# Kernel tuning notes

Measured on AMD Instinct MI355X. Metric: run time of the kernel, lower is better.

The kernel has to match this reference:

```python
import jax, jax.numpy as jnp
import numpy as np

V, E, H, L, B, S = 32000, 512, 512, 2, 8, 512


def setup_inputs() -> dict:
    key = jax.random.key(0)
    ks = jax.random.split(key, 16)
    emb = jax.random.normal(ks[0], (V, E), jnp.float32) * 0.02
    emb = emb.at[0].set(0.0)  # padding_idx=0
    init_state = jax.random.normal(ks[1], (2, L, H), jnp.float32)  # [h;c] params
    def xav(k, shp):
        fan_in, fan_out = shp[1], shp[0]
        lim = np.sqrt(6.0 / (fan_in + fan_out)).astype(np.float32)
        return jax.random.uniform(k, shp, jnp.float32, -lim, lim)
    inp = {
        'emb_table': emb,
        'init_state': init_state,
        'w_ih0': xav(ks[2], (4 * H, E)), 'w_hh0': xav(ks[3], (4 * H, H)),
        'b_ih0': jnp.zeros((4 * H,), jnp.float32), 'b_hh0': jnp.zeros((4 * H,), jnp.float32),
        'w_ih1': xav(ks[4], (4 * H, H)), 'w_hh1': xav(ks[5], (4 * H, H)),
        'b_ih1': jnp.zeros((4 * H,), jnp.float32), 'b_hh1': jnp.zeros((4 * H,), jnp.float32),
        'wg': xav(ks[6], (2 * H, H)), 'bg': jnp.zeros((2 * H,), jnp.float32),
        'wd': xav(ks[7], (V, H)), 'bd': jnp.zeros((V,), jnp.float32),
        'eps': jax.random.normal(ks[8], (B, S, H), jnp.float32),
        'x': jax.random.randint(ks[9], (B, S), 0, V, jnp.int64),
    }
    return inp


def _lstm_layer(xs, h0, c0, w_ih, w_hh, b_ih, b_hh):
    # xs: [S, B, in]; returns hidden sequence [S, B, H]
    b = b_ih + b_hh
    def step(carry, x_t):
        h, c = carry
        gates = x_t @ w_ih.T + h @ w_hh.T + b  # [B, 4H]
        i, f, g, o = jnp.split(gates, 4, axis=-1)  # torch gate order i,f,g,o
        c = jax.nn.sigmoid(f) * c + jax.nn.sigmoid(i) * jnp.tanh(g)
        h = jax.nn.sigmoid(o) * jnp.tanh(c)
        return (h, c), h
    _, hs = jax.lax.scan(step, (h0, c0), xs)
    return hs


def reference(emb_table, init_state, w_ih0, w_hh0, b_ih0, b_hh0,
              w_ih1, w_hh1, b_ih1, b_hh1, wg, bg, wd, bd, eps, x):
    Bsz = x.shape[0]
    embedding = emb_table[x]  # [B, S, E]
    h0 = jnp.broadcast_to(init_state[0][:, None, :], (L, Bsz, H))
    c0 = jnp.broadcast_to(init_state[1][:, None, :], (L, Bsz, H))
    xs = embedding.transpose(1, 0, 2)  # time-major [S, B, E]
    hs0 = _lstm_layer(xs, h0[0], c0[0], w_ih0, w_hh0, b_ih0, b_hh0)
    hs1 = _lstm_layer(hs0, h0[1], c0[1], w_ih1, w_hh1, b_ih1, b_hh1)
    out = hs1.transpose(1, 0, 2)  # [B, S, H]
    stats = out @ wg.T + bg  # [B, S, 2H]
    std = jax.nn.softplus(stats[:, :, :H])  # diagonal of covariance matrix
    mu = stats[:, :, H:]
    # MultivariateNormal(mu, cov=diag(std)).rsample() => mu + sqrt(std) * eps
    sample = mu + jnp.sqrt(std) * eps
    logits = sample @ wd.T + bd  # [B, S, V]
    return (logits, mu, std)
```

## Files before the change

kernel.cpp:

```cpp
#include <hip/hip_runtime.h>


typedef __attribute__((ext_vector_type(4))) float f32x4;
typedef __attribute__((ext_vector_type(8))) short short8;
typedef __attribute__((ext_vector_type(4))) unsigned short u16x4;

#define V_SZ 32000
#define E_SZ 512
#define H_SZ 512
#define B_SZ 8
#define S_SZ 512
#define NTOK 4096
#define G4H  2048

__device__ __forceinline__ unsigned short f2bf(float x) {
  unsigned int b = __float_as_uint(x);
  b += 0x7FFFu + ((b >> 16) & 1u);
  return (unsigned short)(b >> 16);
}
__device__ __forceinline__ float bf2f(unsigned short u) {
  return __uint_as_float(((unsigned int)u) << 16);
}

__device__ __forceinline__ void split4(const f32x4 v, u16x4& hv, u16x4& lv) {
  unsigned short h0 = f2bf(v.x); lv.x = f2bf(v.x - bf2f(h0)); hv.x = h0;
  unsigned short h1 = f2bf(v.y); lv.y = f2bf(v.y - bf2f(h1)); hv.y = h1;
  unsigned short h2 = f2bf(v.z); lv.z = f2bf(v.z - bf2f(h2)); hv.z = h2;
  unsigned short h3 = f2bf(v.w); lv.w = f2bf(v.w - bf2f(h3)); hv.w = h3;
}

__global__ void split_kernel(const float* __restrict__ src,
                             unsigned short* __restrict__ hi,
                             unsigned short* __restrict__ lo, int n4) {
  int i = blockIdx.x * 256 + threadIdx.x;
  if (i >= n4) return;
  f32x4 v = ((const f32x4*)src)[i];
  u16x4 hv, lv;
  split4(v, hv, lv);
  ((u16x4*)hi)[i] = hv;
  ((u16x4*)lo)[i] = lv;
}

__global__ void bias_sum_kernel(const float* __restrict__ a0, const float* __restrict__ c0,
                                const float* __restrict__ a1, const float* __restrict__ c1,
                                float* __restrict__ o0, float* __restrict__ o1) {
  int i = blockIdx.x * 256 + threadIdx.x;
  if (i < G4H) { o0[i] = a0[i] + c0[i]; o1[i] = a1[i] + c1[i]; }
}

__global__ void embed_split_kernel(const float* __restrict__ emb, const int* __restrict__ x,
                                   unsigned short* __restrict__ hi, unsigned short* __restrict__ lo) {
  int gid = blockIdx.x * 256 + threadIdx.x;
  int r = gid >> 7;
  int kq = (gid & 127) << 2;
  int tok = x[r];
  f32x4 v = *(const f32x4*)(emb + (size_t)tok * E_SZ + kq);
  u16x4 hv, lv;
  split4(v, hv, lv);
  *(u16x4*)(hi + (size_t)r * E_SZ + kq) = hv;
  *(u16x4*)(lo + (size_t)r * E_SZ + kq) = lv;
}

__device__ __forceinline__ int swz32(int row, int seg) {
  return row * 32 + (((seg ^ (row & 3)) << 3));
}

__global__ __launch_bounds__(256, 2) void gemm3_kernel(
    const unsigned short* __restrict__ Ah, const unsigned short* __restrict__ Al,
    const unsigned short* __restrict__ Bh, const unsigned short* __restrict__ Bl,
    const float* __restrict__ bias, float* __restrict__ C,
    int M, int N, int K) {
  __shared__ unsigned short sAh[128 * 32];
  __shared__ unsigned short sAl[128 * 32];
  __shared__ unsigned short sBh[128 * 32];
  __shared__ unsigned short sBl[128 * 32];

  const int t = threadIdx.x;
  const int lane = t & 63;
  const int wave = t >> 6;
  const int wr = wave >> 1, wc = wave & 1;
  const size_t m0 = (size_t)blockIdx.y * 128;
  const size_t n0 = (size_t)blockIdx.x * 128;

  f32x4 acc[4][4];
#pragma unroll
  for (int i = 0; i < 4; ++i)
#pragma unroll
    for (int j = 0; j < 4; ++j) acc[i][j] = (f32x4){0.f, 0.f, 0.f, 0.f};

  const int r0 = t >> 2;
  const int seg0 = t & 3;

  const int nk = K >> 5;
  for (int ks = 0; ks < nk; ++ks) {
    const int k0 = ks << 5;
    short8 vAh[2], vAl[2], vBh[2], vBl[2];
#pragma unroll
    for (int r = 0; r < 2; ++r) {
      int row = r0 + r * 64;
      size_t ga = (m0 + row) * (size_t)K + k0 + seg0 * 8;
      size_t gb = (n0 + row) * (size_t)K + k0 + seg0 * 8;
      vAh[r] = *(const short8*)(Ah + ga);
      vAl[r] = *(const short8*)(Al + ga);
      vBh[r] = *(const short8*)(Bh + gb);
      vBl[r] = *(const short8*)(Bl + gb);
    }
    __syncthreads();
#pragma unroll
    for (int r = 0; r < 2; ++r) {
      int row = r0 + r * 64;
      int d = swz32(row, seg0);
      *(short8*)(sAh + d) = vAh[r];
      *(short8*)(sAl + d) = vAl[r];
      *(short8*)(sBh + d) = vBh[r];
      *(short8*)(sBl + d) = vBl[r];
    }
    __syncthreads();

    short8 ah[4], al[4], bh[4], bl[4];
    const int seg = lane >> 4;
#pragma unroll
    for (int m = 0; m < 4; ++m) {
      int row = wr * 64 + m * 16 + (lane & 15);
      int d = swz32(row, seg);
      ah[m] = *(const short8*)(sAh + d);
      al[m] = *(const short8*)(sAl + d);
    }
#pragma unroll
    for (int n = 0; n < 4; ++n) {
      int row = wc * 64 + n * 16 + (lane & 15);
      int d = swz32(row, seg);
      bh[n] = *(const short8*)(sBh + d);
      bl[n] = *(const short8*)(sBl + d);
    }
#pragma unroll
    for (int m = 0; m < 4; ++m) {
#pragma unroll
      for (int n = 0; n < 4; ++n) {
        acc[m][n] = __builtin_amdgcn_mfma_f32_16x16x32_bf16(ah[m], bh[n], acc[m][n], 0, 0, 0);
        acc[m][n] = __builtin_amdgcn_mfma_f32_16x16x32_bf16(ah[m], bl[n], acc[m][n], 0, 0, 0);
        acc[m][n] = __builtin_amdgcn_mfma_f32_16x16x32_bf16(al[m], bh[n], acc[m][n], 0, 0, 0);
      }
    }
  }

#pragma unroll
  for (int m = 0; m < 4; ++m) {
#pragma unroll
    for (int n = 0; n < 4; ++n) {
      size_t gr0 = m0 + wr * 64 + m * 16 + ((lane >> 4) << 2);
      size_t gc = n0 + wc * 64 + n * 16 + (lane & 15);
      float bv = bias ? bias[gc] : 0.f;
#pragma unroll
      for (int j = 0; j < 4; ++j) {
        C[(gr0 + j) * (size_t)N + gc] = acc[m][n][j] + bv;
      }
    }
  }
}

#define SEQ_NB 192
#define SEQ_NB_L0 64

__device__ __forceinline__ float sigm(float x) { return 1.f / (1.f + expf(-x)); }

__global__ __launch_bounds__(256, 1) void lstm_seq_kernel(
    const float* __restrict__ gx0,
    const float* __restrict__ w_hh0,
    const float* __restrict__ w_ih1,
    const float* __restrict__ w_hh1,
    const float* __restrict__ b1s,
    const float* __restrict__ initst,
    float* __restrict__ h0_all,
    float* __restrict__ h1_all,
    unsigned short* __restrict__ hs1h,
    unsigned short* __restrict__ hs1l,
    unsigned int* __restrict__ sig0,
    unsigned int* __restrict__ sig1) {
  const int blk = blockIdx.x;
  const int t = threadIdx.x;
  const bool isL1 = (blk >= SEQ_NB_L0);
  const int lb = isL1 ? (blk - SEQ_NB_L0) : blk;

  __shared__ float hA[8][512];
  __shared__ float hB[8][512];
  __shared__ float gates_s[32][8];

  const int tb = t >> 7;
  const int rg = isL1 ? ((t >> 5) & 3) : ((t >> 4) & 7);
  const int kg = isL1 ? (t & 31) : (t & 15);

  f32x4 w[4][8];
  if (!isL1) {
#pragma unroll
    for (int rr = 0; rr < 4; ++rr) {
      int rl = rg * 4 + rr;
      int grow = (rl >> 3) * H_SZ + lb * 8 + (rl & 7);
      const float* src = w_hh0 + (size_t)grow * H_SZ + kg * 4;
#pragma unroll
      for (int j = 0; j < 8; ++j) w[rr][j] = *(const f32x4*)(src + j * 64);
    }
  } else {
#pragma unroll
    for (int rr = 0; rr < 4; ++rr) {
      int rl = rg * 4 + rr;
      int grow = (rl >> 2) * H_SZ + lb * 4 + (rl & 3);
      const float* s1 = w_ih1 + (size_t)grow * H_SZ + kg * 4;
      const float* s2 = w_hh1 + (size_t)grow * H_SZ + kg * 4;
#pragma unroll
      for (int j = 0; j < 4; ++j) w[rr][j] = *(const f32x4*)(s1 + j * 128);
#pragma unroll
      for (int j = 0; j < 4; ++j) w[rr][4 + j] = *(const f32x4*)(s2 + j * 128);
    }
  }

  const int UPB = isL1 ? 4 : 8;
  const int nCell = UPB * 8;
  const int cu = t >> 3, cb = t & 7;
  const int cunit = lb * UPB + cu;
  float creg = 0.f;
  float bgi = 0.f, bgf = 0.f, bgg = 0.f, bgo = 0.f;
  if (t < nCell) {
    creg = initst[1024 + (isL1 ? 512 : 0) + cunit];
    if (isL1) {
      bgi = b1s[cunit];
      bgf = b1s[512 + cunit];
      bgg = b1s[1024 + cunit];
      bgo = b1s[1536 + cunit];
    }
  }

  for (int step = 0; step < 512; ++step) {
    float pgi = 0.f, pgf = 0.f, pgg = 0.f, pgo = 0.f;
    if (!isL1 && t < nCell) {
      const float* gx = gx0 + ((size_t)(cb * S_SZ + step)) * G4H + cunit;
      pgi = gx[0];
      pgf = gx[512];
      pgg = gx[1024];
      pgo = gx[1536];
    }

    if (t < 64) {
      if (!isL1) {
        if (step > 0) {
          const unsigned int* s0 = sig0 + (size_t)(step - 1) * 64;
          while (true) {
            unsigned int v = __hip_atomic_load(&s0[t], __ATOMIC_RELAXED, __HIP_MEMORY_SCOPE_AGENT);
            if (__all(v != 0)) break;
            __builtin_amdgcn_s_sleep(1);
          }
        }
      } else {
        const unsigned int* s0 = sig0 + (size_t)step * 64;
        const unsigned int* s1 = (step > 0) ? (sig1 + (size_t)(step - 1) * 128) : nullptr;
        while (true) {
          int ok = (__hip_atomic_load(&s0[t], __ATOMIC_RELAXED, __HIP_MEMORY_SCOPE_AGENT) != 0);
          if (s1) {
            ok &= (__hip_atomic_load(&s1[t], __ATOMIC_RELAXED, __HIP_MEMORY_SCOPE_AGENT) != 0);
            ok &= (__hip_atomic_load(&s1[64 + t], __ATOMIC_RELAXED, __HIP_MEMORY_SCOPE_AGENT) != 0);
          }
          if (__all(ok)) break;
          __builtin_amdgcn_s_sleep(1);
        }
      }
    }
    __syncthreads();

    if (!isL1) {
      const float* src = (step == 0) ? (initst) : (h0_all + (size_t)(step - 1) * 4096);
      if (step == 0) {
#pragma unroll
        for (int i = 0; i < 4; ++i) {
          int idx = t + i * 256;
          int b = idx >> 7;
          int kc = (idx & 127) << 2;
          *(f32x4*)&hA[b][kc] = *(const f32x4*)(initst + kc);
        }
      } else {
#pragma unroll
        for (int i = 0; i < 4; ++i) {
          int idx = t + i * 256;
          int b = idx >> 7;
          int kc = (idx & 127) << 2;
          *(f32x4*)&hA[b][kc] = *(const f32x4*)(src + b * H_SZ + kc);
        }
      }
    } else {
      const float* s0 = h0_all + (size_t)step * 4096;
      const float* s1 = (step == 0) ? nullptr : (h1_all + (size_t)(step - 1) * 4096);
#pragma unroll
      for (int i = 0; i < 4; ++i) {
        int idx = t + i * 256;
        int b = idx >> 7;
        int kc = (idx & 127) << 2;
        *(f32x4*)&hA[b][kc] = *(const f32x4*)(s0 + b * H_SZ + kc);
        f32x4 v1 = s1 ? *(const f32x4*)(s1 + b * H_SZ + kc)
                      : *(const f32x4*)(initst + 512 + kc);
        *(f32x4*)&hB[b][kc] = v1;
      }
    }
    __syncthreads();

    float acc[4][4];
#pragma unroll
    for (int rr = 0; rr < 4; ++rr)
#pragma unroll
      for (int bq = 0; bq < 4; ++bq) acc[rr][bq] = 0.f;

    if (!isL1) {
#pragma unroll
      for (int bq = 0; bq < 4; ++bq) {
        const float* hb = &hA[tb * 4 + bq][0];
#pragma unroll
        for (int j = 0; j < 8; ++j) {
          f32x4 hq = *(const f32x4*)(hb + kg * 4 + j * 64);
#pragma unroll
          for (int rr = 0; rr < 4; ++rr)
            acc[rr][bq] += w[rr][j].x * hq.x + w[rr][j].y * hq.y +
                           w[rr][j].z * hq.z + w[rr][j].w * hq.w;
        }
      }
#pragma unroll
      for (int s = 1; s < 16; s <<= 1) {
#pragma unroll
        for (int rr = 0; rr < 4; ++rr)
#pragma unroll
          for (int bq = 0; bq < 4; ++bq)
            acc[rr][bq] += __shfl_xor(acc[rr][bq], s, 64);
      }
      if (kg == 0) {
#pragma unroll
        for (int rr = 0; rr < 4; ++rr)
#pragma unroll
          for (int bq = 0; bq < 4; ++bq)
            gates_s[rg * 4 + rr][tb * 4 + bq] = acc[rr][bq];
      }
    } else {
#pragma unroll
      for (int bq = 0; bq < 4; ++bq) {
        const int b = tb * 4 + bq;
        const float* ha = &hA[b][0];
        const float* hbp = &hB[b][0];
#pragma unroll
        for (int j = 0; j < 4; ++j) {
          f32x4 hq = *(const f32x4*)(ha + kg * 4 + j * 128);
#pragma unroll
          for (int rr = 0; rr < 4; ++rr)
            acc[rr][bq] += w[rr][j].x * hq.x + w[rr][j].y * hq.y +
                           w[rr][j].z * hq.z + w[rr][j].w * hq.w;
        }
#pragma unroll
        for (int j = 0; j < 4; ++j) {
          f32x4 hq = *(const f32x4*)(hbp + kg * 4 + j * 128);
#pragma unroll
          for (int rr = 0; rr < 4; ++rr)
            acc[rr][bq] += w[rr][4 + j].x * hq.x + w[rr][4 + j].y * hq.y +
                           w[rr][4 + j].z * hq.z + w[rr][4 + j].w * hq.w;
        }
      }
#pragma unroll
      for (int s = 1; s < 32; s <<= 1) {
#pragma unroll
        for (int rr = 0; rr < 4; ++rr)
#pragma unroll
          for (int bq = 0; bq < 4; ++bq)
            acc[rr][bq] += __shfl_xor(acc[rr][bq], s, 64);
      }
      if (kg == 0) {
#pragma unroll
        for (int rr = 0; rr < 4; ++rr)
#pragma unroll
          for (int bq = 0; bq < 4; ++bq)
            gates_s[rg * 4 + rr][tb * 4 + bq] = acc[rr][bq];
      }
    }
    __syncthreads();

    if (t < nCell) {
      float gi, gf, gg, go;
      if (!isL1) {
        gi = gates_s[cu][cb] + pgi;
        gf = gates_s[8 + cu][cb] + pgf;
        gg = gates_s[16 + cu][cb] + pgg;
        go = gates_s[24 + cu][cb] + pgo;
      } else {
        gi = gates_s[cu][cb] + bgi;
        gf = gates_s[4 + cu][cb] + bgf;
        gg = gates_s[8 + cu][cb] + bgg;
        go = gates_s[12 + cu][cb] + bgo;
      }
      float cn = sigm(gf) * creg + sigm(gi) * tanhf(gg);
      float h = sigm(go) * tanhf(cn);
      creg = cn;
      if (!isL1) {
        __hip_atomic_store(&h0_all[(size_t)step * 4096 + cb * H_SZ + cunit], h,
                           __ATOMIC_RELAXED, __HIP_MEMORY_SCOPE_AGENT);
      } else {
        __hip_atomic_store(&h1_all[(size_t)step * 4096 + cb * H_SZ + cunit], h,
                           __ATOMIC_RELAXED, __HIP_MEMORY_SCOPE_AGENT);
        size_t r = (size_t)(cb * S_SZ + step) * H_SZ + cunit;
        unsigned short hh = f2bf(h);
        hs1h[r] = hh;
        hs1l[r] = f2bf(h - bf2f(hh));
      }
    }
    if (t == 0) {
      asm volatile("s_waitcnt vmcnt(0)" ::: "memory");
      unsigned int* slot = isL1 ? (sig1 + (size_t)step * 128 + lb)
                                : (sig0 + (size_t)step * 64 + lb);
      __hip_atomic_store(slot, 1u, __ATOMIC_RELAXED, __HIP_MEMORY_SCOPE_AGENT);
    }
  }
}

__global__ void sample_kernel(const float* __restrict__ stats, const float* __restrict__ eps,
                              unsigned short* __restrict__ sh, unsigned short* __restrict__ sl,
                              float* __restrict__ omu, float* __restrict__ ostd) {
  int gid = blockIdx.x * 256 + threadIdx.x;
  int r = gid >> 9, hh = gid & 511;
  float sp = stats[(size_t)r * 1024 + hh];
  float mu = stats[(size_t)r * 1024 + 512 + hh];
  float sd = (sp > 20.f) ? sp : log1pf(expf(sp));
  float smp = mu + sqrtf(sd) * eps[gid];
  omu[gid] = mu;
  ostd[gid] = sd;
  unsigned short h = f2bf(smp);
  sh[gid] = h;
  sl[gid] = f2bf(smp - bf2f(h));
}

extern "C" void kernel_launch(void* const* d_in, const int* in_sizes, int n_in,
                              void* d_out, int out_size, void* d_ws, size_t ws_size,
                              hipStream_t stream) {
  const float* emb    = (const float*)d_in[0];
  const float* initst = (const float*)d_in[1];
  const float* w_ih0  = (const float*)d_in[2];
  const float* w_hh0  = (const float*)d_in[3];
  const float* b_ih0  = (const float*)d_in[4];
  const float* b_hh0  = (const float*)d_in[5];
  const float* w_ih1  = (const float*)d_in[6];
  const float* w_hh1  = (const float*)d_in[7];
  const float* b_ih1  = (const float*)d_in[8];
  const float* b_hh1  = (const float*)d_in[9];
  const float* wg     = (const float*)d_in[10];
  const float* bg     = (const float*)d_in[11];
  const float* wd     = (const float*)d_in[12];
  const float* bd     = (const float*)d_in[13];
  const float* eps    = (const float*)d_in[14];
  const int*   x      = (const int*)d_in[15];

  char* ws = (char*)d_ws;
  size_t off = 0;
  auto alloc = [&](size_t sz) {
    void* p = ws + off;
    off = (off + sz + 255) & ~(size_t)255;
    return p;
  };
  unsigned int* sig0     = (unsigned int*)alloc((size_t)512 * 64 * 4);
  unsigned int* sig1     = (unsigned int*)alloc((size_t)512 * 128 * 4);
  float* b0s             = (float*)alloc(G4H * 4);
  float* b1s             = (float*)alloc(G4H * 4);
  unsigned short* wih0h  = (unsigned short*)alloc((size_t)G4H * E_SZ * 2);
  unsigned short* wih0l  = (unsigned short*)alloc((size_t)G4H * E_SZ * 2);
  unsigned short* wgh    = (unsigned short*)alloc((size_t)1024 * H_SZ * 2);
  unsigned short* wgl    = (unsigned short*)alloc((size_t)1024 * H_SZ * 2);
  unsigned short* wdh    = (unsigned short*)alloc((size_t)V_SZ * H_SZ * 2);
  unsigned short* wdl    = (unsigned short*)alloc((size_t)V_SZ * H_SZ * 2);
  unsigned short* a0h    = (unsigned short*)alloc((size_t)NTOK * E_SZ * 2);
  unsigned short* a0l    = (unsigned short*)alloc((size_t)NTOK * E_SZ * 2);
  float* gx0             = (float*)alloc((size_t)NTOK * G4H * 4);
  float* h0_all          = (float*)alloc((size_t)512 * 4096 * 4);
  float* h1_all          = (float*)alloc((size_t)512 * 4096 * 4);
  unsigned short* hs1h   = (unsigned short*)alloc((size_t)NTOK * H_SZ * 2);
  unsigned short* hs1l   = (unsigned short*)alloc((size_t)NTOK * H_SZ * 2);
  float* stats           = (float*)alloc((size_t)NTOK * 1024 * 4);
  unsigned short* smph   = (unsigned short*)alloc((size_t)NTOK * H_SZ * 2);
  unsigned short* smpl   = (unsigned short*)alloc((size_t)NTOK * H_SZ * 2);

  float* out_logits = (float*)d_out;
  float* out_mu     = out_logits + (size_t)NTOK * V_SZ;
  float* out_std    = out_mu + (size_t)NTOK * H_SZ;

  (void)hipMemsetAsync(sig0, 0, (size_t)512 * 64 * 4, stream);
  (void)hipMemsetAsync(sig1, 0, (size_t)512 * 128 * 4, stream);

  split_kernel<<<(G4H * E_SZ / 4 + 255) / 256, 256, 0, stream>>>(w_ih0, wih0h, wih0l, G4H * E_SZ / 4);
  split_kernel<<<(1024 * H_SZ / 4 + 255) / 256, 256, 0, stream>>>(wg, wgh, wgl, 1024 * H_SZ / 4);
  split_kernel<<<(V_SZ * H_SZ / 4 + 255) / 256, 256, 0, stream>>>(wd, wdh, wdl, V_SZ * H_SZ / 4);
  bias_sum_kernel<<<8, 256, 0, stream>>>(b_ih0, b_hh0, b_ih1, b_hh1, b0s, b1s);

  embed_split_kernel<<<NTOK * 128 / 256, 256, 0, stream>>>(emb, x, a0h, a0l);

  gemm3_kernel<<<dim3(G4H / 128, NTOK / 128), 256, 0, stream>>>(
      a0h, a0l, wih0h, wih0l, b0s, gx0, NTOK, G4H, E_SZ);

  lstm_seq_kernel<<<SEQ_NB, 256, 0, stream>>>(
      gx0, w_hh0, w_ih1, w_hh1, b1s, initst, h0_all, h1_all, hs1h, hs1l, sig0, sig1);

  gemm3_kernel<<<dim3(1024 / 128, NTOK / 128), 256, 0, stream>>>(
      hs1h, hs1l, wgh, wgl, bg, stats, NTOK, 1024, H_SZ);

  sample_kernel<<<NTOK * H_SZ / 256, 256, 0, stream>>>(stats, eps, smph, smpl, out_mu, out_std);

  gemm3_kernel<<<dim3(V_SZ / 128, NTOK / 128), 256, 0, stream>>>(
      smph, smpl, wdh, wdl, bd, out_logits, NTOK, V_SZ, H_SZ);
}
```

Before: 3.789 ms.

## Split layer-1 LSTM into separate input-projection and recurrent block groups

Layer 1 was computed by 128 blocks, each doing both the w_ih1·h0 and w_hh1·h1 products per step. The new scheme uses three groups of 64 blocks: layer-0 recurrence, a layer-1 input-projection group that computes w_ih1·h0[t] as soon as layer 0 finishes step t and publishes the result with per-block flags, and a layer-1 recurrent group that only does w_hh1·h1. This takes the input projection off the layer-1 critical path so it overlaps with the recurrence. The cost is an extra global round trip through gx1 and another level of flag synchronization per step.

```diff
diff --git a/kernel.cpp b/kernel.cpp
--- a/kernel.cpp
+++ b/kernel.cpp
@@ -160,7 +160,6 @@
 }
 
 #define SEQ_NB 192
-#define SEQ_NB_L0 64
 
 __device__ __forceinline__ float sigm(float x) { return 1.f / (1.f + expf(-x)); }
 
@@ -173,56 +172,43 @@
     const float* __restrict__ initst,
     float* __restrict__ h0_all,
     float* __restrict__ h1_all,
+    float* __restrict__ gx1,
     unsigned short* __restrict__ hs1h,
     unsigned short* __restrict__ hs1l,
     unsigned int* __restrict__ sig0,
-    unsigned int* __restrict__ sig1) {
+    unsigned int* __restrict__ sig1,
+    unsigned int* __restrict__ sig1a) {
   const int blk = blockIdx.x;
   const int t = threadIdx.x;
-  const bool isL1 = (blk >= SEQ_NB_L0);
-  const int lb = isL1 ? (blk - SEQ_NB_L0) : blk;
+  const int grp = blk >> 6;
+  const int lb = blk & 63;
 
   __shared__ float hA[8][512];
-  __shared__ float hB[8][512];
   __shared__ float gates_s[32][8];
 
   const int tb = t >> 7;
-  const int rg = isL1 ? ((t >> 5) & 3) : ((t >> 4) & 7);
-  const int kg = isL1 ? (t & 31) : (t & 15);
-
+  const int rg = (t >> 4) & 7;
+  const int kg = t & 15;
+
+  const float* wsrc = (grp == 0) ? w_hh0 : (grp == 1) ? w_ih1 : w_hh1;
   f32x4 w[4][8];
-  if (!isL1) {
-#pragma unroll
-    for (int rr = 0; rr < 4; ++rr) {
-      int rl = rg * 4 + rr;
-      int grow = (rl >> 3) * H_SZ + lb * 8 + (rl & 7);
-      const float* src = w_hh0 + (size_t)grow * H_SZ + kg * 4;
-#pragma unroll
-      for (int j = 0; j < 8; ++j) w[rr][j] = *(const f32x4*)(src + j * 64);
-    }
-  } else {
-#pragma unroll
-    for (int rr = 0; rr < 4; ++rr) {
-      int rl = rg * 4 + rr;
-      int grow = (rl >> 2) * H_SZ + lb * 4 + (rl & 3);
-      const float* s1 = w_ih1 + (size_t)grow * H_SZ + kg * 4;
-      const float* s2 = w_hh1 + (size_t)grow * H_SZ + kg * 4;
-#pragma unroll
-      for (int j = 0; j < 4; ++j) w[rr][j] = *(const f32x4*)(s1 + j * 128);
-#pragma unroll
-      for (int j = 0; j < 4; ++j) w[rr][4 + j] = *(const f32x4*)(s2 + j * 128);
-    }
+#pragma unroll
+  for (int rr = 0; rr < 4; ++rr) {
+    int rl = rg * 4 + rr;
+    int grow = (rl >> 3) * H_SZ + lb * 8 + (rl & 7);
+    const float* src = wsrc + (size_t)grow * H_SZ + kg * 4;
+#pragma unroll
+    for (int j = 0; j < 8; ++j) w[rr][j] = *(const f32x4*)(src + j * 64);
   }
 
-  const int UPB = isL1 ? 4 : 8;
-  const int nCell = UPB * 8;
   const int cu = t >> 3, cb = t & 7;
-  const int cunit = lb * UPB + cu;
+  const int cunit = lb * 8 + cu;
   float creg = 0.f;
   float bgi = 0.f, bgf = 0.f, bgg = 0.f, bgo = 0.f;
-  if (t < nCell) {
-    creg = initst[1024 + (isL1 ? 512 : 0) + cunit];
-    if (isL1) {
+  if (t < 64) {
+    if (grp == 0) creg = initst[1024 + cunit];
+    if (grp == 2) {
+      creg = initst[1024 + 512 + cunit];
       bgi = b1s[cunit];
       bgf = b1s[512 + cunit];
       bgg = b1s[1024 + cunit];
@@ -232,7 +218,7 @@
 
   for (int step = 0; step < 512; ++step) {
     float pgi = 0.f, pgf = 0.f, pgg = 0.f, pgo = 0.f;
-    if (!isL1 && t < nCell) {
+    if (grp == 0 && t < 64) {
       const float* gx = gx0 + ((size_t)(cb * S_SZ + step)) * G4H + cunit;
       pgi = gx[0];
       pgf = gx[512];
@@ -241,7 +227,7 @@
     }
 
     if (t < 64) {
-      if (!isL1) {
+      if (grp == 0) {
         if (step > 0) {
           const unsigned int* s0 = sig0 + (size_t)(step - 1) * 64;
           while (true) {
@@ -250,15 +236,19 @@
             __builtin_amdgcn_s_sleep(1);
           }
         }
+      } else if (grp == 1) {
+        const unsigned int* s0 = sig0 + (size_t)step * 64;
+        while (true) {
+          unsigned int v = __hip_atomic_load(&s0[t], __ATOMIC_RELAXED, __HIP_MEMORY_SCOPE_AGENT);
+          if (__all(v != 0)) break;
+          __builtin_amdgcn_s_sleep(1);
+        }
       } else {
-        const unsigned int* s0 = sig0 + (size_t)step * 64;
-        const unsigned int* s1 = (step > 0) ? (sig1 + (size_t)(step - 1) * 128) : nullptr;
+        const unsigned int* sa = sig1a + (size_t)step * 64 + lb;
+        const unsigned int* s1 = (step > 0) ? (sig1 + (size_t)(step - 1) * 64) : nullptr;
         while (true) {
-          int ok = (__hip_atomic_load(&s0[t], __ATOMIC_RELAXED, __HIP_MEMORY_SCOPE_AGENT) != 0);
-          if (s1) {
-            ok &= (__hip_atomic_load(&s1[t], __ATOMIC_RELAXED, __HIP_MEMORY_SCOPE_AGENT) != 0);
-            ok &= (__hip_atomic_load(&s1[64 + t], __ATOMIC_RELAXED, __HIP_MEMORY_SCOPE_AGENT) != 0);
-          }
+          int ok = (__hip_atomic_load(sa, __ATOMIC_RELAXED, __HIP_MEMORY_SCOPE_AGENT) != 0);
+          if (s1) ok &= (__hip_atomic_load(&s1[t], __ATOMIC_RELAXED, __HIP_MEMORY_SCOPE_AGENT) != 0);
           if (__all(ok)) break;
           __builtin_amdgcn_s_sleep(1);
         }
@@ -266,17 +256,19 @@
     }
     __syncthreads();
 
-    if (!isL1) {
-      const float* src = (step == 0) ? (initst) : (h0_all + (size_t)(step - 1) * 4096);
-      if (step == 0) {
-#pragma unroll
-        for (int i = 0; i < 4; ++i) {
-          int idx = t + i * 256;
-          int b = idx >> 7;
-          int kc = (idx & 127) << 2;
-          *(f32x4*)&hA[b][kc] = *(const f32x4*)(initst + kc);
-        }
-      } else {
+    float gxv[4];
+    if (grp == 2 && t < 64) {
+      const float* gp = gx1 + ((size_t)step * 64 + lb) * 256;
+#pragma unroll
+      for (int g = 0; g < 4; ++g) gxv[g] = gp[(g * 8 + cu) * 8 + cb];
+    }
+
+    {
+      const float* src;
+      if (grp == 0)       src = (step == 0) ? nullptr : (h0_all + (size_t)(step - 1) * 4096);
+      else if (grp == 1)  src = h0_all + (size_t)step * 4096;
+      else                src = (step == 0) ? nullptr : (h1_all + (size_t)(step - 1) * 4096);
+      if (src) {
 #pragma unroll
         for (int i = 0; i < 4; ++i) {
           int idx = t + i * 256;
@@ -284,50 +276,67 @@
           int kc = (idx & 127) << 2;
           *(f32x4*)&hA[b][kc] = *(const f32x4*)(src + b * H_SZ + kc);
         }
-      }
+      } else {
+        const float* ini = initst + (grp == 0 ? 0 : 512);
+#pragma unroll
+        for (int i = 0; i < 4; ++i) {
+          int idx = t + i * 256;
+          int b = idx >> 7;
+          int kc = (idx & 127) << 2;
+          *(f32x4*)&hA[b][kc] = *(const f32x4*)(ini + kc);
+        }
+      }
+    }
+    __syncthreads();
+
+    float acc[4][4];
+#pragma unroll
+    for (int rr = 0; rr < 4; ++rr)
+#pragma unroll
+      for (int bq = 0; bq < 4; ++bq) acc[rr][bq] = 0.f;
+#pragma unroll
+    for (int bq = 0; bq < 4; ++bq) {
+      const float* hb = &hA[tb * 4 + bq][0];
+#pragma unroll
+      for (int j = 0; j < 8; ++j) {
+        f32x4 hq = *(const f32x4*)(hb + kg * 4 + j * 64);
+#pragma unroll
+        for (int rr = 0; rr < 4; ++rr)
+          acc[rr][bq] += w[rr][j].x * hq.x + w[rr][j].y * hq.y +
+                         w[rr][j].z * hq.z + w[rr][j].w * hq.w;
+      }
+    }
+#pragma unroll
+    for (int s = 1; s < 16; s <<= 1) {
+#pragma unroll
+      for (int rr = 0; rr < 4; ++rr)
+#pragma unroll
+        for (int bq = 0; bq < 4; ++bq)
+          acc[rr][bq] += __shfl_xor(acc[rr][bq], s, 64);
+    }
+
+    if (grp == 1) {
+      if (kg == 0) {
+        unsigned long long* gq =
+            (unsigned long long*)(gx1 + ((size_t)step * 64 + lb) * 256);
+#pragma unroll
+        for (int rr = 0; rr < 4; ++rr) {
+          int rl = rg * 4 + rr;
+          unsigned long long lo =
+              ((unsigned long long)__float_as_uint(acc[rr][1]) << 32) |
+              (unsigned long long)__float_as_uint(acc[rr][0]);
+          unsigned long long hi =
+              ((unsigned long long)__float_as_uint(acc[rr][3]) << 32) |
+              (unsigned long long)__float_as_uint(acc[rr][2]);
+          __hip_atomic_store(&gq[rl * 4 + tb * 2], lo, __ATOMIC_RELAXED, __HIP_MEMORY_SCOPE_AGENT);
+          __hip_atomic_store(&gq[rl * 4 + tb * 2 + 1], hi, __ATOMIC_RELAXED, __HIP_MEMORY_SCOPE_AGENT);
+        }
+      }
+      __syncthreads();
+      if (t == 0)
+        __hip_atomic_store(&sig1a[(size_t)step * 64 + lb], 1u,
+                           __ATOMIC_RELAXED, __HIP_MEMORY_SCOPE_AGENT);
     } else {
-      const float* s0 = h0_all + (size_t)step * 4096;
-      const float* s1 = (step == 0) ? nullptr : (h1_all + (size_t)(step - 1) * 4096);
-#pragma unroll
-      for (int i = 0; i < 4; ++i) {
-        int idx = t + i * 256;
-        int b = idx >> 7;
-        int kc = (idx & 127) << 2;
-        *(f32x4*)&hA[b][kc] = *(const f32x4*)(s0 + b * H_SZ + kc);
-        f32x4 v1 = s1 ? *(const f32x4*)(s1 + b * H_SZ + kc)
-                      : *(const f32x4*)(initst + 512 + kc);
-        *(f32x4*)&hB[b][kc] = v1;
-      }
-    }
-    __syncthreads();
-
-    float acc[4][4];
-#pragma unroll
-    for (int rr = 0; rr < 4; ++rr)
-#pragma unroll
-      for (int bq = 0; bq < 4; ++bq) acc[rr][bq] = 0.f;
-
-    if (!isL1) {
-#pragma unroll
-      for (int bq = 0; bq < 4; ++bq) {
-        const float* hb = &hA[tb * 4 + bq][0];
-#pragma unroll
-        for (int j = 0; j < 8; ++j) {
-          f32x4 hq = *(const f32x4*)(hb + kg * 4 + j * 64);
-#pragma unroll
-          for (int rr = 0; rr < 4; ++rr)
-            acc[rr][bq] += w[rr][j].x * hq.x + w[rr][j].y * hq.y +
-                           w[rr][j].z * hq.z + w[rr][j].w * hq.w;
-        }
-      }
-#pragma unroll
-      for (int s = 1; s < 16; s <<= 1) {
-#pragma unroll
-        for (int rr = 0; rr < 4; ++rr)
-#pragma unroll
-          for (int bq = 0; bq < 4; ++bq)
-            acc[rr][bq] += __shfl_xor(acc[rr][bq], s, 64);
-      }
       if (kg == 0) {
 #pragma unroll
         for (int rr = 0; rr < 4; ++rr)
@@ -335,80 +344,42 @@
           for (int bq = 0; bq < 4; ++bq)
             gates_s[rg * 4 + rr][tb * 4 + bq] = acc[rr][bq];
       }
-    } else {
-#pragma unroll
-      for (int bq = 0; bq < 4; ++bq) {
-        const int b = tb * 4 + bq;
-        const float* ha = &hA[b][0];
-        const float* hbp = &hB[b][0];
-#pragma unroll
-        for (int j = 0; j < 4; ++j) {
-          f32x4 hq = *(const f32x4*)(ha + kg * 4 + j * 128);
-#pragma unroll
-          for (int rr = 0; rr < 4; ++rr)
-            acc[rr][bq] += w[rr][j].x * hq.x + w[rr][j].y * hq.y +
-                           w[rr][j].z * hq.z + w[rr][j].w * hq.w;
-        }
-#pragma unroll
-        for (int j = 0; j < 4; ++j) {
-          f32x4 hq = *(const f32x4*)(hbp + kg * 4 + j * 128);
-#pragma unroll
-          for (int rr = 0; rr < 4; ++rr)
-            acc[rr][bq] += w[rr][4 + j].x * hq.x + w[rr][4 + j].y * hq.y +
-                           w[rr][4 + j].z * hq.z + w[rr][4 + j].w * hq.w;
-        }
-      }
-#pragma unroll
-      for (int s = 1; s < 32; s <<= 1) {
-#pragma unroll
-        for (int rr = 0; rr < 4; ++rr)
-#pragma unroll
-          for (int bq = 0; bq < 4; ++bq)
-            acc[rr][bq] += __shfl_xor(acc[rr][bq], s, 64);
-      }
-      if (kg == 0) {
-#pragma unroll
-        for (int rr = 0; rr < 4; ++rr)
-#pragma unroll
-          for (int bq = 0; bq < 4; ++bq)
-            gates_s[rg * 4 + rr][tb * 4 + bq] = acc[rr][bq];
-      }
-    }
-    __syncthreads();
-
-    if (t < nCell) {
-      float gi, gf, gg, go;
-      if (!isL1) {
-        gi = gates_s[cu][cb] + pgi;
-        gf = gates_s[8 + cu][cb] + pgf;
-        gg = gates_s[16 + cu][cb] + pgg;
-        go = gates_s[24 + cu][cb] + pgo;
-      } else {
-        gi = gates_s[cu][cb] + bgi;
-        gf = gates_s[4 + cu][cb] + bgf;
-        gg = gates_s[8 + cu][cb] + bgg;
-        go = gates_s[12 + cu][cb] + bgo;
-      }
-      float cn = sigm(gf) * creg + sigm(gi) * tanhf(gg);
-      float h = sigm(go) * tanhf(cn);
-      creg = cn;
-      if (!isL1) {
-        __hip_atomic_store(&h0_all[(size_t)step * 4096 + cb * H_SZ + cunit], h,
-                           __ATOMIC_RELAXED, __HIP_MEMORY_SCOPE_AGENT);
-      } else {
-        __hip_atomic_store(&h1_all[(size_t)step * 4096 + cb * H_SZ + cunit], h,
-                           __ATOMIC_RELAXED, __HIP_MEMORY_SCOPE_AGENT);
-        size_t r = (size_t)(cb * S_SZ + step) * H_SZ + cunit;
-        unsigned short hh = f2bf(h);
-        hs1h[r] = hh;
-        hs1l[r] = f2bf(h - bf2f(hh));
-      }
-    }
-    if (t == 0) {
-      asm volatile("s_waitcnt vmcnt(0)" ::: "memory");
-      unsigned int* slot = isL1 ? (sig1 + (size_t)step * 128 + lb)
-                                : (sig0 + (size_t)step * 64 + lb);
-      __hip_atomic_store(slot, 1u, __ATOMIC_RELAXED, __HIP_MEMORY_SCOPE_AGENT);
+      __syncthreads();
+
+      if (t < 64) {
+        float gi, gf, gg, go;
+        if (grp == 0) {
+          gi = gates_s[cu][cb] + pgi;
+          gf = gates_s[8 + cu][cb] + pgf;
+          gg = gates_s[16 + cu][cb] + pgg;
+          go = gates_s[24 + cu][cb] + pgo;
+        } else {
+          gi = gates_s[cu][cb] + gxv[0] + bgi;
+          gf = gates_s[8 + cu][cb] + gxv[1] + bgf;
+          gg = gates_s[16 + cu][cb] + gxv[2] + bgg;
+          go = gates_s[24 + cu][cb] + gxv[3] + bgo;
+        }
+        float cn = sigm(gf) * creg + sigm(gi) * tanhf(gg);
+        float h = sigm(go) * tanhf(cn);
+        creg = cn;
+        if (grp == 0) {
+          __hip_atomic_store(&h0_all[(size_t)step * 4096 + cb * H_SZ + cunit], h,
+                             __ATOMIC_RELAXED, __HIP_MEMORY_SCOPE_AGENT);
+        } else {
+          __hip_atomic_store(&h1_all[(size_t)step * 4096 + cb * H_SZ + cunit], h,
+                             __ATOMIC_RELAXED, __HIP_MEMORY_SCOPE_AGENT);
+          size_t r = (size_t)(cb * S_SZ + step) * H_SZ + cunit;
+          unsigned short hh = f2bf(h);
+          hs1h[r] = hh;
+          hs1l[r] = f2bf(h - bf2f(hh));
+        }
+      }
+      if (t == 0) {
+        asm volatile("s_waitcnt vmcnt(0)" ::: "memory");
+        unsigned int* slot = (grp == 0) ? (sig0 + (size_t)step * 64 + lb)
+                                        : (sig1 + (size_t)step * 64 + lb);
+        __hip_atomic_store(slot, 1u, __ATOMIC_RELAXED, __HIP_MEMORY_SCOPE_AGENT);
+      }
     }
   }
 }
@@ -457,7 +428,8 @@
     return p;
   };
   unsigned int* sig0     = (unsigned int*)alloc((size_t)512 * 64 * 4);
-  unsigned int* sig1     = (unsigned int*)alloc((size_t)512 * 128 * 4);
+  unsigned int* sig1     = (unsigned int*)alloc((size_t)512 * 64 * 4);
+  unsigned int* sig1a    = (unsigned int*)alloc((size_t)512 * 64 * 4);
   float* b0s             = (float*)alloc(G4H * 4);
   float* b1s             = (float*)alloc(G4H * 4);
   unsigned short* wih0h  = (unsigned short*)alloc((size_t)G4H * E_SZ * 2);
@@ -469,6 +441,7 @@
   unsigned short* a0h    = (unsigned short*)alloc((size_t)NTOK * E_SZ * 2);
   unsigned short* a0l    = (unsigned short*)alloc((size_t)NTOK * E_SZ * 2);
   float* gx0             = (float*)alloc((size_t)NTOK * G4H * 4);
+  float* gx1             = (float*)alloc((size_t)512 * 64 * 256 * 4);
   float* h0_all          = (float*)alloc((size_t)512 * 4096 * 4);
   float* h1_all          = (float*)alloc((size_t)512 * 4096 * 4);
   unsigned short* hs1h   = (unsigned short*)alloc((size_t)NTOK * H_SZ * 2);
@@ -482,7 +455,8 @@
   float* out_std    = out_mu + (size_t)NTOK * H_SZ;
 
   (void)hipMemsetAsync(sig0, 0, (size_t)512 * 64 * 4, stream);
-  (void)hipMemsetAsync(sig1, 0, (size_t)512 * 128 * 4, stream);
+  (void)hipMemsetAsync(sig1, 0, (size_t)512 * 64 * 4, stream);
+  (void)hipMemsetAsync(sig1a, 0, (size_t)512 * 64 * 4, stream);
 
   split_kernel<<<(G4H * E_SZ / 4 + 255) / 256, 256, 0, stream>>>(w_ih0, wih0h, wih0l, G4H * E_SZ / 4);
   split_kernel<<<(1024 * H_SZ / 4 + 255) / 256, 256, 0, stream>>>(wg, wgh, wgl, 1024 * H_SZ / 4);
@@ -495,7 +469,8 @@
       a0h, a0l, wih0h, wih0l, b0s, gx0, NTOK, G4H, E_SZ);
 
   lstm_seq_kernel<<<SEQ_NB, 256, 0, stream>>>(
-      gx0, w_hh0, w_ih1, w_hh1, b1s, initst, h0_all, h1_all, hs1h, hs1l, sig0, sig1);
+      gx0, w_hh0, w_ih1, w_hh1, b1s, initst, h0_all, h1_all, gx1,
+      hs1h, hs1l, sig0, sig1, sig1a);
 
   gemm3_kernel<<<dim3(1024 / 128, NTOK / 128), 256, 0, stream>>>(
       hs1h, hs1l, wgh, wgl, bg, stats, NTOK, 1024, H_SZ);
```

Measured after the change: 4.185 ms. 10.4% more time.

## Split LSTM layer signals, poll in parallel waves, pack hidden stores

Applied to the files above, without the earlier changes.

Layer-0 step flags are duplicated into two arrays, one polled by layer-0 blocks and one by layer-1 blocks, so the two groups do not contend on the same cache lines. Layer-1 blocks now poll the layer-0 flags and the two halves of the layer-1 flags from three separate wavefronts instead of one wave checking all three. Hidden-state stores are packed into 64-bit atomics via a lane shuffle, and the bf16 split writes for hs1 are moved after the signal so they leave the recurrent critical path. The aim is lower per-step cross-block synchronisation latency in the sequential LSTM, at the cost of an extra flag array and memset.

```diff
diff --git a/kernel.cpp b/kernel.cpp
--- a/kernel.cpp
+++ b/kernel.cpp
@@ -175,12 +175,15 @@
     float* __restrict__ h1_all,
     unsigned short* __restrict__ hs1h,
     unsigned short* __restrict__ hs1l,
-    unsigned int* __restrict__ sig0,
+    unsigned int* __restrict__ sig0a,
+    unsigned int* __restrict__ sig0b,
     unsigned int* __restrict__ sig1) {
   const int blk = blockIdx.x;
   const int t = threadIdx.x;
   const bool isL1 = (blk >= SEQ_NB_L0);
   const int lb = isL1 ? (blk - SEQ_NB_L0) : blk;
+  const int lane = t & 63;
+  const int wv = t >> 6;
 
   __shared__ float hA[8][512];
   __shared__ float hB[8][512];
@@ -240,49 +243,51 @@
       pgo = gx[1536];
     }
 
-    if (t < 64) {
-      if (!isL1) {
-        if (step > 0) {
-          const unsigned int* s0 = sig0 + (size_t)(step - 1) * 64;
-          while (true) {
-            unsigned int v = __hip_atomic_load(&s0[t], __ATOMIC_RELAXED, __HIP_MEMORY_SCOPE_AGENT);
-            if (__all(v != 0)) break;
-            __builtin_amdgcn_s_sleep(1);
-          }
+    if (!isL1) {
+      if (t < 64 && step > 0) {
+        const unsigned int* s0 = sig0a + (size_t)(step - 1) * 64;
+        while (true) {
+          unsigned int v = __hip_atomic_load(&s0[t], __ATOMIC_RELAXED, __HIP_MEMORY_SCOPE_AGENT);
+          if (__all(v != 0)) break;
+          __builtin_amdgcn_s_sleep(1);
+        }
+      }
+    } else {
+      if (wv == 0) {
+        const unsigned int* s0 = sig0b + (size_t)step * 64;
+        while (true) {
+          unsigned int v = __hip_atomic_load(&s0[lane], __ATOMIC_RELAXED, __HIP_MEMORY_SCOPE_AGENT);
+          if (__all(v != 0)) break;
+          __builtin_amdgcn_s_sleep(1);
+        }
+      } else if ((wv == 1 || wv == 2) && step > 0) {
+        const unsigned int* s1 = sig1 + (size_t)(step - 1) * 128 + (wv - 1) * 64;
+        while (true) {
+          unsigned int v = __hip_atomic_load(&s1[lane], __ATOMIC_RELAXED, __HIP_MEMORY_SCOPE_AGENT);
+          if (__all(v != 0)) break;
+          __builtin_amdgcn_s_sleep(1);
+        }
+      }
+    }
+    __syncthreads();
+
+    if (!isL1) {
+      const float* src = (step == 0) ? nullptr : (h0_all + (size_t)(step - 1) * 4096);
+      if (src) {
+#pragma unroll
+        for (int i = 0; i < 4; ++i) {
+          int idx = t + i * 256;
+          int b = idx >> 7;
+          int kc = (idx & 127) << 2;
+          *(f32x4*)&hA[b][kc] = *(const f32x4*)(src + b * H_SZ + kc);
         }
       } else {
-        const unsigned int* s0 = sig0 + (size_t)step * 64;
-        const unsigned int* s1 = (step > 0) ? (sig1 + (size_t)(step - 1) * 128) : nullptr;
-        while (true) {
-          int ok = (__hip_atomic_load(&s0[t], __ATOMIC_RELAXED, __HIP_MEMORY_SCOPE_AGENT) != 0);
-          if (s1) {
-            ok &= (__hip_atomic_load(&s1[t], __ATOMIC_RELAXED, __HIP_MEMORY_SCOPE_AGENT) != 0);
-            ok &= (__hip_atomic_load(&s1[64 + t], __ATOMIC_RELAXED, __HIP_MEMORY_SCOPE_AGENT) != 0);
-          }
-          if (__all(ok)) break;
-          __builtin_amdgcn_s_sleep(1);
-        }
-      }
-    }
-    __syncthreads();
-
-    if (!isL1) {
-      const float* src = (step == 0) ? (initst) : (h0_all + (size_t)(step - 1) * 4096);
-      if (step == 0) {
 #pragma unroll
         for (int i = 0; i < 4; ++i) {
           int idx = t + i * 256;
           int b = idx >> 7;
           int kc = (idx & 127) << 2;
           *(f32x4*)&hA[b][kc] = *(const f32x4*)(initst + kc);
-        }
-      } else {
-#pragma unroll
-        for (int i = 0; i < 4; ++i) {
-          int idx = t + i * 256;
-          int b = idx >> 7;
-          int kc = (idx & 127) << 2;
-          *(f32x4*)&hA[b][kc] = *(const f32x4*)(src + b * H_SZ + kc);
         }
       }
     } else {
@@ -376,6 +381,7 @@
     }
     __syncthreads();
 
+    float hval = 0.f;
     if (t < nCell) {
       float gi, gf, gg, go;
       if (!isL1) {
@@ -390,25 +396,36 @@
         go = gates_s[12 + cu][cb] + bgo;
       }
       float cn = sigm(gf) * creg + sigm(gi) * tanhf(gg);
-      float h = sigm(go) * tanhf(cn);
+      hval = sigm(go) * tanhf(cn);
       creg = cn;
+      float hp = __shfl_xor(hval, 8, 64);
+      if ((t & 8) == 0) {
+        float* hbase = isL1 ? h1_all : h0_all;
+        unsigned long long pk =
+            ((unsigned long long)__float_as_uint(hp) << 32) |
+            (unsigned long long)__float_as_uint(hval);
+        unsigned long long* dst = (unsigned long long*)
+            (hbase + (size_t)step * 4096 + cb * H_SZ + cunit);
+        __hip_atomic_store(dst, pk, __ATOMIC_RELAXED, __HIP_MEMORY_SCOPE_AGENT);
+      }
+    }
+    if (t == 0) {
+      asm volatile("s_waitcnt vmcnt(0)" ::: "memory");
       if (!isL1) {
-        __hip_atomic_store(&h0_all[(size_t)step * 4096 + cb * H_SZ + cunit], h,
+        __hip_atomic_store(&sig0a[(size_t)step * 64 + lb], 1u,
+                           __ATOMIC_RELAXED, __HIP_MEMORY_SCOPE_AGENT);
+        __hip_atomic_store(&sig0b[(size_t)step * 64 + lb], 1u,
                            __ATOMIC_RELAXED, __HIP_MEMORY_SCOPE_AGENT);
       } else {
-        __hip_atomic_store(&h1_all[(size_t)step * 4096 + cb * H_SZ + cunit], h,
+        __hip_atomic_store(&sig1[(size_t)step * 128 + lb], 1u,
                            __ATOMIC_RELAXED, __HIP_MEMORY_SCOPE_AGENT);
-        size_t r = (size_t)(cb * S_SZ + step) * H_SZ + cunit;
-        unsigned short hh = f2bf(h);
-        hs1h[r] = hh;
-        hs1l[r] = f2bf(h - bf2f(hh));
-      }
-    }
-    if (t == 0) {
-      asm volatile("s_waitcnt vmcnt(0)" ::: "memory");
-      unsigned int* slot = isL1 ? (sig1 + (size_t)step * 128 + lb)
-                                : (sig0 + (size_t)step * 64 + lb);
-      __hip_atomic_store(slot, 1u, __ATOMIC_RELAXED, __HIP_MEMORY_SCOPE_AGENT);
+      }
+    }
+    if (isL1 && t < nCell) {
+      size_t r = (size_t)(cb * S_SZ + step) * H_SZ + cunit;
+      unsigned short hh = f2bf(hval);
+      hs1h[r] = hh;
+      hs1l[r] = f2bf(hval - bf2f(hh));
     }
   }
 }
@@ -456,7 +473,8 @@
     off = (off + sz + 255) & ~(size_t)255;
     return p;
   };
-  unsigned int* sig0     = (unsigned int*)alloc((size_t)512 * 64 * 4);
+  unsigned int* sig0a    = (unsigned int*)alloc((size_t)512 * 64 * 4);
+  unsigned int* sig0b    = (unsigned int*)alloc((size_t)512 * 64 * 4);
   unsigned int* sig1     = (unsigned int*)alloc((size_t)512 * 128 * 4);
   float* b0s             = (float*)alloc(G4H * 4);
   float* b1s             = (float*)alloc(G4H * 4);
@@ -481,7 +499,8 @@
   float* out_mu     = out_logits + (size_t)NTOK * V_SZ;
   float* out_std    = out_mu + (size_t)NTOK * H_SZ;
 
-  (void)hipMemsetAsync(sig0, 0, (size_t)512 * 64 * 4, stream);
+  (void)hipMemsetAsync(sig0a, 0, (size_t)512 * 64 * 4, stream);
+  (void)hipMemsetAsync(sig0b, 0, (size_t)512 * 64 * 4, stream);
   (void)hipMemsetAsync(sig1, 0, (size_t)512 * 128 * 4, stream);
 
   split_kernel<<<(G4H * E_SZ / 4 + 255) / 256, 256, 0, stream>>>(w_ih0, wih0h, wih0l, G4H * E_SZ / 4);
@@ -495,7 +514,8 @@
       a0h, a0l, wih0h, wih0l, b0s, gx0, NTOK, G4H, E_SZ);
 
   lstm_seq_kernel<<<SEQ_NB, 256, 0, stream>>>(
-      gx0, w_hh0, w_ih1, w_hh1, b1s, initst, h0_all, h1_all, hs1h, hs1l, sig0, sig1);
+      gx0, w_hh0, w_ih1, w_hh1, b1s, initst, h0_all, h1_all,
+      hs1h, hs1l, sig0a, sig0b, sig1);
 
   gemm3_kernel<<<dim3(1024 / 128, NTOK / 128), 256, 0, stream>>>(
       hs1h, hs1l, wgh, wgl, bg, stats, NTOK, 1024, H_SZ);
```

Result: slower. 4.858 ms (+28.2%).
